# Optimization experiments

Measured on AMD Instinct MI355X. Metric: run time of the kernel, lower is better.

The kernel has to match this reference:

```python
import jax, jax.numpy as jnp
import numpy as np

B, S, D, H = 2, 2048, 1024, 16  # batch, seq, embed_dim, num_heads
DH = D // H                      # head dim = 64


def setup_inputs() -> dict:
    key = jax.random.key(0)
    kx, kq, kbq, kk, kbk, kv, kbv = jax.random.split(key, 7)
    scale = 1.0 / np.sqrt(D)
    return {
        "x": jax.random.normal(kx, (B, S, D), dtype=jnp.float32),
        "Wq": jax.random.normal(kq, (D, D), dtype=jnp.float32) * scale,
        "bq": jax.random.normal(kbq, (D,), dtype=jnp.float32) * 0.01,
        "Wk": jax.random.normal(kk, (D, D), dtype=jnp.float32) * scale,
        "bk": jax.random.normal(kbk, (D,), dtype=jnp.float32) * 0.01,
        "Wv": jax.random.normal(kv, (D, D), dtype=jnp.float32) * scale,
        "bv": jax.random.normal(kbv, (D,), dtype=jnp.float32) * 0.01,
    }


def reference(x, Wq, bq, Wk, bk, Wv, bv):
    # ooqkv_type == 'q', odeint_method == 'id': q branch = act(Linear(x)), exact GELU (torch nn.GELU default)
    q = jax.nn.gelu(x @ Wq + bq, approximate=False)
    k = x @ Wk + bk
    v = x @ Wv + bv
    # [B, S, D] -> [B, S, H, DH]
    q = q.reshape(B, S, H, DH)
    k = k.reshape(B, S, H, DH)
    v = v.reshape(B, S, H, DH)
    # NOTE: original module has NO 1/sqrt(d) scale — faithful reproduction
    att = jnp.einsum("bqhd,bkhd->bhqk", q, k)
    att = jax.nn.softmax(att, axis=-1)
    out = jnp.einsum("bhqk,bkhd->bqhd", att, v)
    return out.reshape(B, S, D)
```

## Files before the change

kernel.cpp:

```cpp
#include <hip/hip_runtime.h>
#include <math.h>

#define B_  2
#define S_  2048
#define D_  1024
#define H_  16
#define DH_ 64
#define M_  (B_ * S_)

typedef _Float16 half_t;
typedef __attribute__((ext_vector_type(8))) _Float16 h8;
typedef __attribute__((ext_vector_type(4))) _Float16 h4;
typedef __attribute__((ext_vector_type(4))) float   f32x4;

#define LOG2E 1.44269504088896f

__device__ __forceinline__ void gll16(const half_t* g, half_t* l) {
    __builtin_amdgcn_global_load_lds(
        (__attribute__((address_space(1))) const void*)g,
        (__attribute__((address_space(3))) void*)l, 16, 0, 0);
}

__global__ __launch_bounds__(256) void prep_k(
    const float* __restrict__ x, half_t* __restrict__ xh,
    const float* __restrict__ Wq, const float* __restrict__ Wk,
    const float* __restrict__ Wv, half_t* __restrict__ Wt)
{
    const int bx = blockIdx.x;
    if (bx < 2048) {
        const size_t i = ((size_t)bx * 256 + threadIdx.x) * 8;
        const float4 a = *(const float4*)(x + i);
        const float4 b = *(const float4*)(x + i + 4);
        h8 o;
        o[0] = (half_t)a.x; o[1] = (half_t)a.y; o[2] = (half_t)a.z; o[3] = (half_t)a.w;
        o[4] = (half_t)b.x; o[5] = (half_t)b.y; o[6] = (half_t)b.z; o[7] = (half_t)b.w;
        *(h8*)(xh + i) = o;
    } else {
        const int gb    = bx - 2048;
        const int which = gb >> 9;
        const float* __restrict__ W = (which == 0) ? Wq : (which == 1) ? Wk : Wv;
        half_t* __restrict__ T = Wt + (size_t)which * D_ * D_;
        const int gw   = (gb & 511) * 4 + (threadIdx.x >> 6);
        const int lane = threadIdx.x & 63;
        const int n    = (gw & 15) * 64 + lane;
        const int k0   = (gw >> 4) * 8;
        h8 o;
        #pragma unroll
        for (int t = 0; t < 8; ++t) o[t] = (half_t)W[(size_t)(k0 + t) * D_ + n];
        *(h8*)(T + (size_t)n * D_ + k0) = o;
    }
}

__global__ __launch_bounds__(256) void qkv_gemm_f16(
    const half_t* __restrict__ xh, const half_t* __restrict__ Wt,
    const float* __restrict__ bq, const float* __restrict__ bk,
    const float* __restrict__ bv,
    half_t* __restrict__ Qo, half_t* __restrict__ Ko, half_t* __restrict__ Vt)
{
    const int bi = blockIdx.x;
    const int mt = (bi & 7) * 4 + ((bi >> 3) & 3);
    const int nt = bi >> 5;
    const int m0 = mt * 128;
    const int n0g = nt * 128;
    const int which = n0g >> 10;
    const int n0    = n0g & 1023;
    const half_t* __restrict__ Wp  = Wt + (size_t)which * D_ * D_;
    const float* __restrict__ bias = (which == 0) ? bq : (which == 1) ? bk : bv;

    const int tid = threadIdx.x, lane = tid & 63, wave = tid >> 6;
    const int wm = (wave >> 1) * 64, wn = (wave & 1) * 64;
    const int ln = lane & 15, quad = lane >> 4;

    __shared__ __align__(16) half_t As[128 * 64];
    __shared__ __align__(16) half_t Bs[128 * 64];

    f32x4 acc[4][4];
    #pragma unroll
    for (int i = 0; i < 4; ++i)
        #pragma unroll
        for (int j = 0; j < 4; ++j) acc[i][j] = (f32x4){0.f, 0.f, 0.f, 0.f};

    for (int k0 = 0; k0 < D_; k0 += 64) {
        __syncthreads();
        #pragma unroll
        for (int l = 0; l < 4; ++l) {
            const int c  = tid + l * 256;
            const int r  = c >> 3, c0 = c & 7;
            const int cs = c0 ^ (r & 7);
            gll16(xh + (size_t)(m0 + r) * D_ + k0 + cs * 8, &As[c * 8]);
            gll16(Wp + (size_t)(n0 + r) * D_ + k0 + cs * 8, &Bs[c * 8]);
        }
        __syncthreads();

        #pragma unroll
        for (int kc = 0; kc < 2; ++kc) {
            h8 af[4], bf[4];
            #pragma unroll
            for (int i = 0; i < 4; ++i) {
                const int r = wm + i * 16 + ln;
                af[i] = *(const h8*)&As[r * 64 + (((kc << 2) + quad) ^ (r & 7)) * 8];
            }
            #pragma unroll
            for (int j = 0; j < 4; ++j) {
                const int r = wn + j * 16 + ln;
                bf[j] = *(const h8*)&Bs[r * 64 + (((kc << 2) + quad) ^ (r & 7)) * 8];
            }
            #pragma unroll
            for (int i = 0; i < 4; ++i)
                #pragma unroll
                for (int j = 0; j < 4; ++j)
                    acc[i][j] = __builtin_amdgcn_mfma_f32_16x16x32_f16(
                        af[i], bf[j], acc[i][j], 0, 0, 0);
        }
    }

    if (which == 2) {
        #pragma unroll
        for (int j = 0; j < 4; ++j) {
            const int col = n0 + wn + j * 16 + ln;
            const int h = col >> 6, d = col & 63;
            const float bb = bias[col];
            #pragma unroll
            for (int i = 0; i < 4; ++i) {
                const int sg = m0 + wm + i * 16 + quad * 4;
                const int b  = sg >> 11, srow = sg & 2047;
                h4 pv;
                #pragma unroll
                for (int r = 0; r < 4; ++r) pv[r] = (half_t)(acc[i][j][r] + bb);
                *(h4*)(Vt + (((size_t)(b * H_ + h) * DH_ + d) * S_ + srow)) = pv;
            }
        }
    } else {
        half_t* __restrict__ out = (which == 0) ? Qo : Ko;
        #pragma unroll
        for (int j = 0; j < 4; ++j) {
            const int col = n0 + wn + j * 16 + ln;
            const float bb = bias[col];
            #pragma unroll
            for (int i = 0; i < 4; ++i) {
                #pragma unroll
                for (int r = 0; r < 4; ++r) {
                    const int row = m0 + wm + i * 16 + quad * 4 + r;
                    float t = acc[i][j][r] + bb;
                    if (which == 0) {
                        const float u = t * fmaf(t * t, 0.0356774081f, 0.7978845608f);
                        const float e = __builtin_amdgcn_exp2f(u * -2.88539008178f);
                        t = t * __builtin_amdgcn_rcpf(1.0f + e) * LOG2E;
                    }
                    out[(size_t)row * D_ + col] = (half_t)t;
                }
            }
        }
    }
}

__global__ __launch_bounds__(128) void attn_f16(
    const half_t* __restrict__ Q, const half_t* __restrict__ K,
    const half_t* __restrict__ Vt, float* __restrict__ out)
{
    const int tid  = threadIdx.x;
    const int lane = tid & 63;
    const int wave = tid >> 6;
    const int ln   = lane & 15;
    const int quad = lane >> 4;

    const int bi = blockIdx.x;
    const int bh = (bi & 7) * 4 + ((bi >> 3) & 3);
    const int q0 = (bi >> 5) * 64;
    const int b  = bh >> 4;
    const int h  = bh & 15;

    const half_t* __restrict__ Qb  = Q  + (size_t)b * S_ * D_ + h * DH_;
    const half_t* __restrict__ Kb  = K  + (size_t)b * S_ * D_ + h * DH_;
    const half_t* __restrict__ Vtb = Vt + (size_t)bh * DH_ * S_;

    __shared__ __align__(16) half_t Ks[64 * 64];
    __shared__ __align__(16) half_t Vs[64 * 64];
    __shared__ __align__(16) half_t Ps[64][72];

    const int qra = q0 + wave * 32 + ln;
    const h8 qa0 = *(const h8*)(Qb + (size_t)qra * D_ + quad * 8);
    const h8 qa1 = *(const h8*)(Qb + (size_t)qra * D_ + 32 + quad * 8);
    const h8 qc0 = *(const h8*)(Qb + (size_t)(qra + 16) * D_ + quad * 8);
    const h8 qc1 = *(const h8*)(Qb + (size_t)(qra + 16) * D_ + 32 + quad * 8);

    h8 ones8;
    #pragma unroll
    for (int t = 0; t < 8; ++t) ones8[t] = (half_t)1.0f;

    f32x4 Oa[4], Ob[4];
    #pragma unroll
    for (int j = 0; j < 4; ++j) {
        Oa[j] = (f32x4){0.f, 0.f, 0.f, 0.f};
        Ob[j] = (f32x4){0.f, 0.f, 0.f, 0.f};
    }
    f32x4 la = (f32x4){0.f, 0.f, 0.f, 0.f};
    f32x4 lb = (f32x4){0.f, 0.f, 0.f, 0.f};
    float m_a = -INFINITY, m_b = -INFINITY;

    for (int k0 = 0; k0 < S_; k0 += 64) {
        __syncthreads();
        #pragma unroll
        for (int l = 0; l < 4; ++l) {
            const int c  = tid + l * 128;
            const int r  = c >> 3, c0 = c & 7;
            const int cs = c0 ^ (r & 7);
            gll16(Kb  + (size_t)(k0 + r) * D_ + cs * 8, &Ks[c * 8]);
            gll16(Vtb + (size_t)r * S_ + k0 + cs * 8,   &Vs[c * 8]);
        }
        __syncthreads();

        f32x4 sa[4], sb[4];
        #pragma unroll
        for (int j = 0; j < 4; ++j) {
            const int rK = j * 16 + ln;
            const h8 ka0 = *(const h8*)&Ks[rK * 64 + ((quad)     ^ (rK & 7)) * 8];
            const h8 ka1 = *(const h8*)&Ks[rK * 64 + ((quad + 4) ^ (rK & 7)) * 8];
            f32x4 t = (f32x4){0.f, 0.f, 0.f, 0.f};
            t = __builtin_amdgcn_mfma_f32_16x16x32_f16(ka0, qa0, t, 0, 0, 0);
            t = __builtin_amdgcn_mfma_f32_16x16x32_f16(ka1, qa1, t, 0, 0, 0);
            sa[j] = t;
            f32x4 u = (f32x4){0.f, 0.f, 0.f, 0.f};
            u = __builtin_amdgcn_mfma_f32_16x16x32_f16(ka0, qc0, u, 0, 0, 0);
            u = __builtin_amdgcn_mfma_f32_16x16x32_f16(ka1, qc1, u, 0, 0, 0);
            sb[j] = u;
        }

        float mxa = sa[0][0], mxb = sb[0][0];
        #pragma unroll
        for (int j = 0; j < 4; ++j)
            #pragma unroll
            for (int r = 0; r < 4; ++r) {
                mxa = fmaxf(mxa, sa[j][r]);
                mxb = fmaxf(mxb, sb[j][r]);
            }
        mxa = fmaxf(mxa, __shfl_xor(mxa, 16, 64));
        mxa = fmaxf(mxa, __shfl_xor(mxa, 32, 64));
        mxb = fmaxf(mxb, __shfl_xor(mxb, 16, 64));
        mxb = fmaxf(mxb, __shfl_xor(mxb, 32, 64));

        if (__ballot(mxa > m_a || mxb > m_b)) {
            const float mna = fmaxf(m_a, mxa);
            const float mnb = fmaxf(m_b, mxb);
            const float ala = __builtin_amdgcn_exp2f(m_a - mna);
            const float alb = __builtin_amdgcn_exp2f(m_b - mnb);
            m_a = mna; m_b = mnb;
            float ra[4], rb[4];
            #pragma unroll
            for (int r = 0; r < 4; ++r) {
                ra[r] = __shfl(ala, quad * 4 + r, 64);
                rb[r] = __shfl(alb, quad * 4 + r, 64);
            }
            #pragma unroll
            for (int r = 0; r < 4; ++r) {
                la[r] *= ra[r]; lb[r] *= rb[r];
                #pragma unroll
                for (int j = 0; j < 4; ++j) { Oa[j][r] *= ra[r]; Ob[j][r] *= rb[r]; }
            }
        }

        #pragma unroll
        for (int j = 0; j < 4; ++j) {
            h4 pva, pvb;
            #pragma unroll
            for (int r = 0; r < 4; ++r) {
                pva[r] = (half_t)__builtin_amdgcn_exp2f(sa[j][r] - m_a);
                pvb[r] = (half_t)__builtin_amdgcn_exp2f(sb[j][r] - m_b);
            }
            *(h4*)&Ps[wave * 32 + ln][j * 16 + quad * 4]      = pva;
            *(h4*)&Ps[wave * 32 + 16 + ln][j * 16 + quad * 4] = pvb;
        }

        const h8 pa0 = *(const h8*)&Ps[wave * 32 + ln][quad * 8];
        const h8 pa1 = *(const h8*)&Ps[wave * 32 + ln][32 + quad * 8];
        const h8 pb0 = *(const h8*)&Ps[wave * 32 + 16 + ln][quad * 8];
        const h8 pb1 = *(const h8*)&Ps[wave * 32 + 16 + ln][32 + quad * 8];
        #pragma unroll
        for (int j = 0; j < 4; ++j) {
            const int rV = j * 16 + ln;
            const h8 vb0 = *(const h8*)&Vs[rV * 64 + ((quad)     ^ (rV & 7)) * 8];
            const h8 vb1 = *(const h8*)&Vs[rV * 64 + ((quad + 4) ^ (rV & 7)) * 8];
            Oa[j] = __builtin_amdgcn_mfma_f32_16x16x32_f16(pa0, vb0, Oa[j], 0, 0, 0);
            Oa[j] = __builtin_amdgcn_mfma_f32_16x16x32_f16(pa1, vb1, Oa[j], 0, 0, 0);
            Ob[j] = __builtin_amdgcn_mfma_f32_16x16x32_f16(pb0, vb0, Ob[j], 0, 0, 0);
            Ob[j] = __builtin_amdgcn_mfma_f32_16x16x32_f16(pb1, vb1, Ob[j], 0, 0, 0);
        }
        la = __builtin_amdgcn_mfma_f32_16x16x32_f16(pa0, ones8, la, 0, 0, 0);
        la = __builtin_amdgcn_mfma_f32_16x16x32_f16(pa1, ones8, la, 0, 0, 0);
        lb = __builtin_amdgcn_mfma_f32_16x16x32_f16(pb0, ones8, lb, 0, 0, 0);
        lb = __builtin_amdgcn_mfma_f32_16x16x32_f16(pb1, ones8, lb, 0, 0, 0);
    }

    #pragma unroll
    for (int r = 0; r < 4; ++r) {
        const float iva = 1.0f / la[r];
        const float ivb = 1.0f / lb[r];
        const int rowa = q0 + wave * 32 + quad * 4 + r;
        const int rowb = rowa + 16;
        #pragma unroll
        for (int j = 0; j < 4; ++j) {
            out[((size_t)b * S_ + rowa) * D_ + h * DH_ + j * 16 + ln] = Oa[j][r] * iva;
            out[((size_t)b * S_ + rowb) * D_ + h * DH_ + j * 16 + ln] = Ob[j][r] * ivb;
        }
    }
}

extern "C" void kernel_launch(void* const* d_in, const int* in_sizes, int n_in,
                              void* d_out, int out_size, void* d_ws, size_t ws_size,
                              hipStream_t stream) {
    const float* x  = (const float*)d_in[0];
    const float* Wq = (const float*)d_in[1];
    const float* bq = (const float*)d_in[2];
    const float* Wk = (const float*)d_in[3];
    const float* bk = (const float*)d_in[4];
    const float* Wv = (const float*)d_in[5];
    const float* bv = (const float*)d_in[6];
    float* out = (float*)d_out;

    const size_t nmd = (size_t)M_ * D_;
    const size_t ndd = (size_t)D_ * D_;
    half_t* xh  = (half_t*)d_ws;
    half_t* Wt  = xh + nmd;
    half_t* Qh  = Wt + 3 * ndd;
    half_t* Kh  = Qh + nmd;
    half_t* Vtw = Kh + nmd;

    prep_k<<<2048 + 1536, 256, 0, stream>>>(x, xh, Wq, Wk, Wv, Wt);
    qkv_gemm_f16<<<768, 256, 0, stream>>>(xh, Wt, bq, bk, bv, Qh, Kh, Vtw);
    attn_f16<<<1024, 128, 0, stream>>>(Qh, Kh, Vtw, out);
}
```

Baseline: 199.8 us.

## Double-buffer LDS tiles in QKV GEMM and attention kernels

Both the projection GEMM and the attention kernel now keep two LDS buffers. Each loop iteration issues the async global-to-LDS loads for the next tile right after a single barrier, then computes on the current tile, so the load latency overlaps with MFMA work and one barrier per iteration is removed. In the GEMM the K-step shrinks to 32, which means more iterations, and the XOR swizzle on the LDS layout is dropped, which may add bank conflicts. The attention kernel roughly doubles its K/V LDS footprint, which could lower occupancy.

```diff
diff --git a/kernel.cpp b/kernel.cpp
--- a/kernel.cpp
+++ b/kernel.cpp
@@ -71,8 +71,8 @@
     const int wm = (wave >> 1) * 64, wn = (wave & 1) * 64;
     const int ln = lane & 15, quad = lane >> 4;
 
-    __shared__ __align__(16) half_t As[128 * 64];
-    __shared__ __align__(16) half_t Bs[128 * 64];
+    __shared__ __align__(16) half_t As[2][128 * 32];
+    __shared__ __align__(16) half_t Bs[2][128 * 32];
 
     f32x4 acc[4][4];
     #pragma unroll
@@ -80,38 +80,43 @@
         #pragma unroll
         for (int j = 0; j < 4; ++j) acc[i][j] = (f32x4){0.f, 0.f, 0.f, 0.f};
 
-    for (int k0 = 0; k0 < D_; k0 += 64) {
+    {
+        #pragma unroll
+        for (int l = 0; l < 2; ++l) {
+            const int c = tid + l * 256;
+            const int r = c >> 2, c8 = c & 3;
+            gll16(xh + (size_t)(m0 + r) * D_ + c8 * 8, &As[0][c * 8]);
+            gll16(Wp + (size_t)(n0 + r) * D_ + c8 * 8, &Bs[0][c * 8]);
+        }
+    }
+
+    for (int kt = 0; kt < 32; ++kt) {
         __syncthreads();
-        #pragma unroll
-        for (int l = 0; l < 4; ++l) {
-            const int c  = tid + l * 256;
-            const int r  = c >> 3, c0 = c & 7;
-            const int cs = c0 ^ (r & 7);
-            gll16(xh + (size_t)(m0 + r) * D_ + k0 + cs * 8, &As[c * 8]);
-            gll16(Wp + (size_t)(n0 + r) * D_ + k0 + cs * 8, &Bs[c * 8]);
-        }
-        __syncthreads();
-
-        #pragma unroll
-        for (int kc = 0; kc < 2; ++kc) {
-            h8 af[4], bf[4];
-            #pragma unroll
-            for (int i = 0; i < 4; ++i) {
-                const int r = wm + i * 16 + ln;
-                af[i] = *(const h8*)&As[r * 64 + (((kc << 2) + quad) ^ (r & 7)) * 8];
-            }
-            #pragma unroll
-            for (int j = 0; j < 4; ++j) {
-                const int r = wn + j * 16 + ln;
-                bf[j] = *(const h8*)&Bs[r * 64 + (((kc << 2) + quad) ^ (r & 7)) * 8];
-            }
-            #pragma unroll
-            for (int i = 0; i < 4; ++i)
-                #pragma unroll
-                for (int j = 0; j < 4; ++j)
-                    acc[i][j] = __builtin_amdgcn_mfma_f32_16x16x32_f16(
-                        af[i], bf[j], acc[i][j], 0, 0, 0);
-        }
+        if (kt + 1 < 32) {
+            const int k0 = (kt + 1) * 32;
+            const int pb = (kt + 1) & 1;
+            #pragma unroll
+            for (int l = 0; l < 2; ++l) {
+                const int c = tid + l * 256;
+                const int r = c >> 2, c8 = c & 3;
+                gll16(xh + (size_t)(m0 + r) * D_ + k0 + c8 * 8, &As[pb][c * 8]);
+                gll16(Wp + (size_t)(n0 + r) * D_ + k0 + c8 * 8, &Bs[pb][c * 8]);
+            }
+        }
+        const int p = kt & 1;
+        h8 af[4], bf[4];
+        #pragma unroll
+        for (int i = 0; i < 4; ++i)
+            af[i] = *(const h8*)&As[p][(wm + i * 16 + ln) * 32 + quad * 8];
+        #pragma unroll
+        for (int j = 0; j < 4; ++j)
+            bf[j] = *(const h8*)&Bs[p][(wn + j * 16 + ln) * 32 + quad * 8];
+        #pragma unroll
+        for (int i = 0; i < 4; ++i)
+            #pragma unroll
+            for (int j = 0; j < 4; ++j)
+                acc[i][j] = __builtin_amdgcn_mfma_f32_16x16x32_f16(
+                    af[i], bf[j], acc[i][j], 0, 0, 0);
     }
 
     if (which == 2) {
@@ -174,8 +179,8 @@
     const half_t* __restrict__ Kb  = K  + (size_t)b * S_ * D_ + h * DH_;
     const half_t* __restrict__ Vtb = Vt + (size_t)bh * DH_ * S_;
 
-    __shared__ __align__(16) half_t Ks[64 * 64];
-    __shared__ __align__(16) half_t Vs[64 * 64];
+    __shared__ __align__(16) half_t Ks[2][64 * 64];
+    __shared__ __align__(16) half_t Vs[2][64 * 64];
     __shared__ __align__(16) half_t Ps[64][72];
 
     const int qra = q0 + wave * 32 + ln;
@@ -198,28 +203,41 @@
     f32x4 lb = (f32x4){0.f, 0.f, 0.f, 0.f};
     float m_a = -INFINITY, m_b = -INFINITY;
 
-    for (int k0 = 0; k0 < S_; k0 += 64) {
+    #pragma unroll
+    for (int l = 0; l < 4; ++l) {
+        const int c  = tid + l * 128;
+        const int r  = c >> 3, c0 = c & 7;
+        const int cs = c0 ^ (r & 7);
+        gll16(Kb  + (size_t)r * D_ + cs * 8, &Ks[0][c * 8]);
+        gll16(Vtb + (size_t)r * S_ + cs * 8, &Vs[0][c * 8]);
+    }
+
+    for (int t = 0; t < 32; ++t) {
         __syncthreads();
-        #pragma unroll
-        for (int l = 0; l < 4; ++l) {
-            const int c  = tid + l * 128;
-            const int r  = c >> 3, c0 = c & 7;
-            const int cs = c0 ^ (r & 7);
-            gll16(Kb  + (size_t)(k0 + r) * D_ + cs * 8, &Ks[c * 8]);
-            gll16(Vtb + (size_t)r * S_ + k0 + cs * 8,   &Vs[c * 8]);
-        }
-        __syncthreads();
+        if (t + 1 < 32) {
+            const int k0 = (t + 1) * 64;
+            const int pb = (t + 1) & 1;
+            #pragma unroll
+            for (int l = 0; l < 4; ++l) {
+                const int c  = tid + l * 128;
+                const int r  = c >> 3, c0 = c & 7;
+                const int cs = c0 ^ (r & 7);
+                gll16(Kb  + (size_t)(k0 + r) * D_ + cs * 8, &Ks[pb][c * 8]);
+                gll16(Vtb + (size_t)r * S_ + k0 + cs * 8,   &Vs[pb][c * 8]);
+            }
+        }
+        const int p = t & 1;
 
         f32x4 sa[4], sb[4];
         #pragma unroll
         for (int j = 0; j < 4; ++j) {
             const int rK = j * 16 + ln;
-            const h8 ka0 = *(const h8*)&Ks[rK * 64 + ((quad)     ^ (rK & 7)) * 8];
-            const h8 ka1 = *(const h8*)&Ks[rK * 64 + ((quad + 4) ^ (rK & 7)) * 8];
-            f32x4 t = (f32x4){0.f, 0.f, 0.f, 0.f};
-            t = __builtin_amdgcn_mfma_f32_16x16x32_f16(ka0, qa0, t, 0, 0, 0);
-            t = __builtin_amdgcn_mfma_f32_16x16x32_f16(ka1, qa1, t, 0, 0, 0);
-            sa[j] = t;
+            const h8 ka0 = *(const h8*)&Ks[p][rK * 64 + ((quad)     ^ (rK & 7)) * 8];
+            const h8 ka1 = *(const h8*)&Ks[p][rK * 64 + ((quad + 4) ^ (rK & 7)) * 8];
+            f32x4 tt = (f32x4){0.f, 0.f, 0.f, 0.f};
+            tt = __builtin_amdgcn_mfma_f32_16x16x32_f16(ka0, qa0, tt, 0, 0, 0);
+            tt = __builtin_amdgcn_mfma_f32_16x16x32_f16(ka1, qa1, tt, 0, 0, 0);
+            sa[j] = tt;
             f32x4 u = (f32x4){0.f, 0.f, 0.f, 0.f};
             u = __builtin_amdgcn_mfma_f32_16x16x32_f16(ka0, qc0, u, 0, 0, 0);
             u = __builtin_amdgcn_mfma_f32_16x16x32_f16(ka1, qc1, u, 0, 0, 0);
@@ -278,8 +296,8 @@
         #pragma unroll
         for (int j = 0; j < 4; ++j) {
             const int rV = j * 16 + ln;
-            const h8 vb0 = *(const h8*)&Vs[rV * 64 + ((quad)     ^ (rV & 7)) * 8];
-            const h8 vb1 = *(const h8*)&Vs[rV * 64 + ((quad + 4) ^ (rV & 7)) * 8];
+            const h8 vb0 = *(const h8*)&Vs[p][rV * 64 + ((quad)     ^ (rV & 7)) * 8];
+            const h8 vb1 = *(const h8*)&Vs[p][rV * 64 + ((quad + 4) ^ (rV & 7)) * 8];
             Oa[j] = __builtin_amdgcn_mfma_f32_16x16x32_f16(pa0, vb0, Oa[j], 0, 0, 0);
             Oa[j] = __builtin_amdgcn_mfma_f32_16x16x32_f16(pa1, vb1, Oa[j], 0, 0, 0);
             Ob[j] = __builtin_amdgcn_mfma_f32_16x16x32_f16(pb0, vb0, Ob[j], 0, 0, 0);
```

Result: slower. 252.8 us (+26.5%).

## Split attention over key halves and merge partial results in a combine kernel

Applied to the files above, without the earlier changes.

The attention kernel now splits the key dimension into two halves (split-K / flash-decoding style). This doubles the grid to 2048 blocks of 128 threads, which is meant to fill more of the GPU. Each split writes unnormalized partial outputs plus row sum and max, and a new combine kernel rescales and merges them. Separately, the weight-transpose prep now maps its threads differently so that reads along n are coalesced. The cost is extra fp32 partial-output traffic and one more kernel launch.

```diff
diff --git a/kernel.cpp b/kernel.cpp
--- a/kernel.cpp
+++ b/kernel.cpp
@@ -36,18 +36,21 @@
         o[4] = (half_t)b.x; o[5] = (half_t)b.y; o[6] = (half_t)b.z; o[7] = (half_t)b.w;
         *(h8*)(xh + i) = o;
     } else {
-        const int gb    = bx - 2048;
-        const int which = gb >> 9;
+        const int gwv   = (bx - 2048) * 4 + (threadIdx.x >> 6);
+        const int which = gwv >> 11;
         const float* __restrict__ W = (which == 0) ? Wq : (which == 1) ? Wk : Wv;
         half_t* __restrict__ T = Wt + (size_t)which * D_ * D_;
-        const int gw   = (gb & 511) * 4 + (threadIdx.x >> 6);
+        const int t    = gwv & 2047;
+        const int n0   = (t & 127) * 8;
+        const int k0   = (t >> 7) * 64;
         const int lane = threadIdx.x & 63;
-        const int n    = (gw & 15) * 64 + lane;
-        const int k0   = (gw >> 4) * 8;
+        const int kc   = lane & 7, nn = lane >> 3;
+        const int n    = n0 + nn;
         h8 o;
         #pragma unroll
-        for (int t = 0; t < 8; ++t) o[t] = (half_t)W[(size_t)(k0 + t) * D_ + n];
-        *(h8*)(T + (size_t)n * D_ + k0) = o;
+        for (int i = 0; i < 8; ++i)
+            o[i] = (half_t)W[(size_t)(k0 + kc * 8 + i) * D_ + n];
+        *(h8*)(T + (size_t)n * D_ + k0 + kc * 8) = o;
     }
 }
 
@@ -156,7 +159,8 @@
 
 __global__ __launch_bounds__(128) void attn_f16(
     const half_t* __restrict__ Q, const half_t* __restrict__ K,
-    const half_t* __restrict__ Vt, float* __restrict__ out)
+    const half_t* __restrict__ Vt, float* __restrict__ O0,
+    float* __restrict__ O1, float* __restrict__ Lm)
 {
     const int tid  = threadIdx.x;
     const int lane = tid & 63;
@@ -164,15 +168,19 @@
     const int ln   = lane & 15;
     const int quad = lane >> 4;
 
-    const int bi = blockIdx.x;
-    const int bh = (bi & 7) * 4 + ((bi >> 3) & 3);
-    const int q0 = (bi >> 5) * 64;
-    const int b  = bh >> 4;
-    const int h  = bh & 15;
+    const int bi   = blockIdx.x;
+    const int bh   = (bi & 7) * 4 + ((bi >> 3) & 3);
+    const int rest = bi >> 5;
+    const int q0   = (rest & 31) * 64;
+    const int sp   = rest >> 5;
+    const int b    = bh >> 4;
+    const int h    = bh & 15;
+    const int kbase = sp * (S_ / 2);
 
     const half_t* __restrict__ Qb  = Q  + (size_t)b * S_ * D_ + h * DH_;
     const half_t* __restrict__ Kb  = K  + (size_t)b * S_ * D_ + h * DH_;
     const half_t* __restrict__ Vtb = Vt + (size_t)bh * DH_ * S_;
+    float* __restrict__ Op = sp ? O1 : O0;
 
     __shared__ __align__(16) half_t Ks[64 * 64];
     __shared__ __align__(16) half_t Vs[64 * 64];
@@ -198,7 +206,8 @@
     f32x4 lb = (f32x4){0.f, 0.f, 0.f, 0.f};
     float m_a = -INFINITY, m_b = -INFINITY;
 
-    for (int k0 = 0; k0 < S_; k0 += 64) {
+    for (int t = 0; t < 16; ++t) {
+        const int k0 = kbase + t * 64;
         __syncthreads();
         #pragma unroll
         for (int l = 0; l < 4; ++l) {
@@ -216,10 +225,10 @@
             const int rK = j * 16 + ln;
             const h8 ka0 = *(const h8*)&Ks[rK * 64 + ((quad)     ^ (rK & 7)) * 8];
             const h8 ka1 = *(const h8*)&Ks[rK * 64 + ((quad + 4) ^ (rK & 7)) * 8];
-            f32x4 t = (f32x4){0.f, 0.f, 0.f, 0.f};
-            t = __builtin_amdgcn_mfma_f32_16x16x32_f16(ka0, qa0, t, 0, 0, 0);
-            t = __builtin_amdgcn_mfma_f32_16x16x32_f16(ka1, qa1, t, 0, 0, 0);
-            sa[j] = t;
+            f32x4 tt = (f32x4){0.f, 0.f, 0.f, 0.f};
+            tt = __builtin_amdgcn_mfma_f32_16x16x32_f16(ka0, qa0, tt, 0, 0, 0);
+            tt = __builtin_amdgcn_mfma_f32_16x16x32_f16(ka1, qa1, tt, 0, 0, 0);
+            sa[j] = tt;
             f32x4 u = (f32x4){0.f, 0.f, 0.f, 0.f};
             u = __builtin_amdgcn_mfma_f32_16x16x32_f16(ka0, qc0, u, 0, 0, 0);
             u = __builtin_amdgcn_mfma_f32_16x16x32_f16(ka1, qc1, u, 0, 0, 0);
@@ -291,18 +300,64 @@
         lb = __builtin_amdgcn_mfma_f32_16x16x32_f16(pb1, ones8, lb, 0, 0, 0);
     }
 
+    float mra[4], mrb[4];
     #pragma unroll
     for (int r = 0; r < 4; ++r) {
-        const float iva = 1.0f / la[r];
-        const float ivb = 1.0f / lb[r];
+        mra[r] = __shfl(m_a, quad * 4 + r, 64);
+        mrb[r] = __shfl(m_b, quad * 4 + r, 64);
+    }
+    #pragma unroll
+    for (int r = 0; r < 4; ++r) {
         const int rowa = q0 + wave * 32 + quad * 4 + r;
         const int rowb = rowa + 16;
         #pragma unroll
         for (int j = 0; j < 4; ++j) {
-            out[((size_t)b * S_ + rowa) * D_ + h * DH_ + j * 16 + ln] = Oa[j][r] * iva;
-            out[((size_t)b * S_ + rowb) * D_ + h * DH_ + j * 16 + ln] = Ob[j][r] * ivb;
-        }
-    }
+            Op[((size_t)b * S_ + rowa) * D_ + h * DH_ + j * 16 + ln] = Oa[j][r];
+            Op[((size_t)b * S_ + rowb) * D_ + h * DH_ + j * 16 + ln] = Ob[j][r];
+        }
+    }
+    if (ln == 0) {
+        float* Lp = Lm + (size_t)(sp * 32 + bh) * S_;
+        float* Mp = Lp + 2 * 32 * S_;
+        #pragma unroll
+        for (int r = 0; r < 4; ++r) {
+            const int rowa = q0 + wave * 32 + quad * 4 + r;
+            Lp[rowa]      = la[r];  Mp[rowa]      = mra[r];
+            Lp[rowa + 16] = lb[r];  Mp[rowa + 16] = mrb[r];
+        }
+    }
+}
+
+__global__ __launch_bounds__(256) void combine_k(
+    float* __restrict__ out, const float* __restrict__ O1,
+    const float* __restrict__ Lm)
+{
+    const size_t u  = (size_t)blockIdx.x * 256 + threadIdx.x;
+    const size_t e  = u * 4;
+    const int rg = (int)(e >> 10);
+    const int c  = (int)(e & 1023);
+    const int h  = c >> 6;
+    const int b  = rg >> 11, s = rg & 2047;
+    const int bh = b * H_ + h;
+
+    const float l0 = Lm[(size_t)bh * S_ + s];
+    const float l1 = Lm[(size_t)(32 + bh) * S_ + s];
+    const float m0 = Lm[(size_t)(64 + bh) * S_ + s];
+    const float m1 = Lm[(size_t)(96 + bh) * S_ + s];
+    const float m  = fmaxf(m0, m1);
+    float w0 = __builtin_amdgcn_exp2f(m0 - m);
+    float w1 = __builtin_amdgcn_exp2f(m1 - m);
+    const float inv = 1.0f / (l0 * w0 + l1 * w1);
+    w0 *= inv; w1 *= inv;
+
+    const float4 a = *(const float4*)(out + e);
+    const float4 d = *(const float4*)(O1 + e);
+    float4 o;
+    o.x = a.x * w0 + d.x * w1;
+    o.y = a.y * w0 + d.y * w1;
+    o.z = a.z * w0 + d.z * w1;
+    o.w = a.w * w0 + d.w * w1;
+    *(float4*)(out + e) = o;
 }
 
 extern "C" void kernel_launch(void* const* d_in, const int* in_sizes, int n_in,
@@ -324,8 +379,11 @@
     half_t* Qh  = Wt + 3 * ndd;
     half_t* Kh  = Qh + nmd;
     half_t* Vtw = Kh + nmd;
+    float*  O1  = (float*)(Vtw + nmd);
+    float*  Lm  = O1 + nmd;
 
     prep_k<<<2048 + 1536, 256, 0, stream>>>(x, xh, Wq, Wk, Wv, Wt);
     qkv_gemm_f16<<<768, 256, 0, stream>>>(xh, Wt, bq, bk, bv, Qh, Kh, Vtw);
-    attn_f16<<<1024, 128, 0, stream>>>(Qh, Kh, Vtw, out);
-}
+    attn_f16<<<2048, 128, 0, stream>>>(Qh, Kh, Vtw, out, O1, Lm);
+    combine_k<<<(int)(nmd / (256 * 4)), 256, 0, stream>>>(out, O1, Lm);
+}
```

Result: slower. 226.8 us (+13.5%).
